# Performance work log

Measured on AMD Instinct MI355X. Metric: run time of the kernel, lower is better.

## Reference

```python
import jax, jax.numpy as jnp
import numpy as np
from jax import lax

LONG_EDGE = 1024
MAX_SIZE = 1333.0
STRIDES = (4, 8, 16, 32, 64)
SIZES = (32, 64, 128, 256, 512)
RATIOS = (0.5, 1.0, 2.0)
PRE_NMS_TOPK = 6000
POST_NMS_TOPK = 1000
NMS_THRESH = 0.7
NUM_CH = 256


def _gen_anchors_level(scale, ratios, shape, stride):
    # faithful copy of generate_anchors_keras (numpy, static)
    scales, ratios = np.meshgrid(np.array([scale], dtype=np.float64), np.array(ratios, dtype=np.float64))
    scales = scales.flatten(); ratios = ratios.flatten()
    size_ratios = stride * stride / ratios
    widths = np.round(np.sqrt(size_ratios))
    heights = np.round(widths * ratios)
    widths = widths * (scales / stride)
    heights = heights * (scales / stride)
    shifts_y = np.arange(0, shape[0]) * stride + (stride - 1) / 2
    shifts_x = np.arange(0, shape[1]) * stride + (stride - 1) / 2
    shifts_x, shifts_y = np.meshgrid(shifts_x, shifts_y)
    box_widths, box_centers_x = np.meshgrid(widths, shifts_x)
    box_heights, box_centers_y = np.meshgrid(heights, shifts_y)
    box_centers = np.stack([box_centers_y, box_centers_x], axis=2).reshape([-1, 2])
    box_sizes = np.stack([box_heights, box_widths], axis=2).reshape([-1, 2])
    boxes = np.concatenate([box_centers - 0.5 * (box_sizes - 1), box_centers + 0.5 * (box_sizes - 1)], axis=1)
    boxes[:, [2, 3]] += 1
    return boxes[:, [1, 0, 3, 2]].astype(np.float32)


def all_anchors():
    shapes = [(int(np.ceil(LONG_EDGE / s)),) * 2 for s in STRIDES]
    return np.concatenate([_gen_anchors_level(SIZES[i], RATIOS, shapes[i], STRIDES[i]) for i in range(len(STRIDES))], axis=0)


def conv2d(x, w, b, padding):
    y = lax.conv_general_dilated(x, w, (1, 1), padding, dimension_numbers=('NCHW', 'OIHW', 'NCHW'))
    return y + b[None, :, None, None]


def decode_bbox_target(deltas, anchors):
    # deltas, anchors: [K,4]
    txty, twth = deltas[:, :2], deltas[:, 2:]
    x1y1, x2y2 = anchors[:, :2], anchors[:, 2:]
    waha = x2y2 - x1y1
    xaya = (x2y2 + x1y1) * 0.5
    clipv = jnp.float32(np.log(MAX_SIZE / 16.0))
    wbhb = jnp.exp(jnp.minimum(twth, clipv)) * waha
    xbyb = txty * waha + xaya
    return jnp.concatenate([xbyb - wbhb * 0.5, xbyb + wbhb * 0.5], axis=1)


def clip_boxes(b, h, w):
    # faithful to source: x clamped to window[0]=h, y to window[1]=w
    return jnp.stack([b[:, 0].clip(0.0, h), b[:, 1].clip(0.0, w), b[:, 2].clip(0.0, h), b[:, 3].clip(0.0, w)], 1)


def nms_keep(boxes, thresh):
    # boxes sorted by descending score; greedy NMS over full IoU matrix
    x1, y1, x2, y2 = boxes[:, 0], boxes[:, 1], boxes[:, 2], boxes[:, 3]
    areas = (x2 - x1) * (y2 - y1)
    iw = jnp.clip(jnp.minimum(x2[:, None], x2[None, :]) - jnp.maximum(x1[:, None], x1[None, :]), 0.0)
    ih = jnp.clip(jnp.minimum(y2[:, None], y2[None, :]) - jnp.maximum(y1[:, None], y1[None, :]), 0.0)
    inter = iw * ih
    iou = inter / (areas[:, None] + areas[None, :] - inter)
    n = boxes.shape[0]
    sup = iou > thresh
    idxs = jnp.arange(n)
    def body(i, keep):
        row = sup[i] & (idxs > i)
        return jnp.where(keep[i], keep & ~row, keep)
    return lax.fori_loop(0, n, body, jnp.ones((n,), bool))


def rpn_forward(image, feats, w0, b0, wcls, bcls, wbox, bbox):
    labels, boxes_l = [], []
    for f in feats:
        hidden = jax.nn.relu(conv2d(f, w0, b0, 'SAME'))
        cls = conv2d(hidden, wcls, bcls, 'VALID')   # [1,A,H,W]
        box = conv2d(hidden, wbox, bbox, 'VALID')   # [1,4A,H,W]
        labels.append(jnp.transpose(cls, (0, 2, 3, 1)).reshape(1, -1, 1))
        boxes_l.append(jnp.transpose(box, (0, 2, 3, 1)).reshape(1, -1, 4))
    scores = jnp.concatenate(labels, axis=1)[0, :, 0]          # [N]
    box_logits = jnp.concatenate(boxes_l, axis=1)[0]           # [N,4]
    anchors = jnp.asarray(all_anchors())                       # [N,4]
    k = min(PRE_NMS_TOPK, anchors.shape[0])
    _, order = lax.top_k(scores, k)
    deltas = box_logits[order]
    pre_anch = anchors[order]
    dec = decode_bbox_target(deltas, pre_anch)
    h, w = float(image.shape[2]), float(image.shape[3])
    boxes = clip_boxes(dec, h, w)
    keep = nms_keep(lax.stop_gradient(boxes), NMS_THRESH)
    sel = jnp.argsort(~keep)[:POST_NMS_TOPK]  # stable: kept boxes in score order, then pad slots
    proposals = jnp.where(keep[sel][:, None], boxes[sel], 0.0)
    return proposals


def setup_inputs() -> dict:
    key = jax.random.key(0)
    ks = jax.random.split(key, 9)
    hw = [256, 128, 64, 32, 16]
    inp = {'image': jax.random.normal(ks[0], (1, 3, 1024, 1024), jnp.float32)}
    for i, s in enumerate(hw):
        inp[f'feat{i}'] = jax.random.normal(jax.random.fold_in(ks[1], i), (1, NUM_CH, s, s), jnp.float32)
    inp['w0'] = jax.random.normal(ks[2], (NUM_CH, NUM_CH, 3, 3), jnp.float32) * 0.01
    inp['b0'] = jnp.zeros((NUM_CH,), jnp.float32)
    inp['wcls'] = jax.random.normal(ks[3], (3, NUM_CH, 1, 1), jnp.float32) * 0.01
    inp['bcls'] = jnp.zeros((3,), jnp.float32)
    inp['wbox'] = jax.random.normal(ks[4], (12, NUM_CH, 1, 1), jnp.float32) * 0.01
    inp['bbox'] = jnp.zeros((12,), jnp.float32)
    return inp


def reference(image, feat0, feat1, feat2, feat3, feat4, w0, b0, wcls, bcls, wbox, bbox):
    feats = [feat0, feat1, feat2, feat3, feat4]
    return rpn_forward(image, feats, w0, b0, wcls, bcls, wbox, bbox)
```

## Files before the change

### kernel.cpp

```cpp
#include <hip/hip_runtime.h>
#include <cstdint>

typedef unsigned long long u64;
typedef unsigned int u32;
typedef unsigned short ushort;
typedef __attribute__((ext_vector_type(8))) short short8;
typedef __attribute__((ext_vector_type(4))) float f32x4;

#define A_TOTAL 261888
#define NPIX    87296
#define KTOP    6000
#define KTARGET 7800
#define NWORDS  94
#define CANDMAX 8192
#define PIXMAX  8192
#define NBINS   16384

__device__ __forceinline__ u64 score_key64(double s) {
  u64 u = (u64)__double_as_longlong(s);
  return (u & 0x8000000000000000ULL) ? ~u : (u | 0x8000000000000000ULL);
}
__device__ __forceinline__ u32 key32(float s) {
  u32 u = __float_as_uint(s);
  return (u & 0x80000000u) ? ~u : (u | 0x80000000u);
}
__device__ __forceinline__ ushort f2bf(float f) {
  u32 u = __float_as_uint(f);
  u32 r = (u + 0x7FFFu + ((u >> 16) & 1u)) >> 16;
  return (ushort)r;
}
__device__ __forceinline__ void pix_level(int pix, int& l, int& off) {
  if (pix < 65536)      { l = 0; off = 0; }
  else if (pix < 81920) { l = 1; off = 65536; }
  else if (pix < 86016) { l = 2; off = 81920; }
  else if (pix < 87040) { l = 3; off = 86016; }
  else                  { l = 4; off = 87040; }
}

__global__ void k_prep_w(const float* __restrict__ w0, double* __restrict__ wt64,
                         ushort* __restrict__ wkf) {
  int i = blockIdx.x * 256 + threadIdx.x;
  if (i < 256 * 2304) {
    int o = i & 255;
    int ictap = i >> 8;
    float v = w0[o * 2304 + ictap];
    wt64[(size_t)ictap * 256 + o] = (double)v;
    int ic = ictap / 9;
    int tap = ictap - ic * 9;
    int w = o >> 6, mt = (o >> 4) & 3, l15 = o & 15;
    int ch = ic >> 5, kk = ic & 31;
    int l4 = kk >> 3, e = kk & 7;
    int lane = l4 * 16 + l15;
    wkf[((((w * 4 + mt) * 8 + ch) * 9 + tap) << 9) + lane * 8 + e] = f2bf(v);
  }
}

__global__ __launch_bounds__(256, 2) void k_conv_mfma(
    const float* __restrict__ f0, const float* __restrict__ f1,
    const float* __restrict__ f2, const float* __restrict__ f3,
    const float* __restrict__ f4,
    const ushort* __restrict__ wkf, const float* __restrict__ b0,
    const float* __restrict__ wcls, const float* __restrict__ bcls,
    float* __restrict__ scr)
{
  __shared__ ushort xsl[100][40];
  __shared__ float  part[3][64][17];

  int b = blockIdx.x;
  int l, tb;
  if (b < 1024)      { l = 0; tb = b; }
  else if (b < 1280) { l = 1; tb = b - 1024; }
  else if (b < 1344) { l = 2; tb = b - 1280; }
  else if (b < 1360) { l = 3; tb = b - 1344; }
  else               { l = 4; tb = b - 1360; }
  const float* feat = (l == 0) ? f0 : (l == 1) ? f1 : (l == 2) ? f2 : (l == 3) ? f3 : f4;
  int Hh = 256 >> l;
  int HW = Hh * Hh;
  int pixOff = (l == 0) ? 0 : (l == 1) ? 65536 : (l == 2) ? 81920 : (l == 3) ? 86016 : 87040;
  int shl = 5 - l;
  int ty = (tb >> shl) << 3;
  int tx = (tb & ((1 << shl) - 1)) << 3;

  int tid = threadIdx.x;
  int w = tid >> 6;
  int lane = tid & 63;
  int l15 = lane & 15;
  int l4 = lane >> 4;

  f32x4 zz = {0.f, 0.f, 0.f, 0.f};
  f32x4 acc[4][4];
  #pragma unroll
  for (int mt = 0; mt < 4; ++mt)
    #pragma unroll
    for (int tt = 0; tt < 4; ++tt) acc[mt][tt] = zz;

  for (int ch = 0; ch < 8; ++ch) {
    __syncthreads();
    for (int e = tid; e < 3200; e += 256) {
      int icl = e / 100;
      int sp = e - icl * 100;
      int yy = sp / 10;
      int xx = sp - yy * 10;
      int gy = ty + yy - 1, gx = tx + xx - 1;
      float v = 0.f;
      if (gy >= 0 && gy < Hh && gx >= 0 && gx < Hh)
        v = feat[(ch * 32 + icl) * HW + gy * Hh + gx];
      xsl[sp][icl] = f2bf(v);
    }
    __syncthreads();
    #pragma unroll
    for (int tap = 0; tap < 9; ++tap) {
      int dy = tap / 3;
      int dx = tap - dy * 3;
      short8 af[4], bf[4];
      #pragma unroll
      for (int mt = 0; mt < 4; ++mt) {
        int abase = ((((w * 4 + mt) * 8 + ch) * 9 + tap) << 9) + (lane << 3);
        af[mt] = *(const short8*)(wkf + abase);
      }
      #pragma unroll
      for (int tt = 0; tt < 4; ++tt) {
        int p = (tt << 4) + l15;
        int sp = ((p >> 3) + dy) * 10 + (p & 7) + dx;
        bf[tt] = *(const short8*)&xsl[sp][l4 << 3];
      }
      #pragma unroll
      for (int mt = 0; mt < 4; ++mt)
        #pragma unroll
        for (int tt = 0; tt < 4; ++tt)
          acc[mt][tt] = __builtin_amdgcn_mfma_f32_16x16x32_bf16(af[mt], bf[tt], acc[mt][tt], 0, 0, 0);
    }
  }

  float pr[3][4];
  #pragma unroll
  for (int kk = 0; kk < 3; ++kk)
    #pragma unroll
    for (int tt = 0; tt < 4; ++tt) pr[kk][tt] = 0.f;
  #pragma unroll
  for (int mt = 0; mt < 4; ++mt) {
    #pragma unroll
    for (int r = 0; r < 4; ++r) {
      int oc = (w << 6) + (mt << 4) + (l4 << 2) + r;
      float bb = b0[oc];
      float c0 = wcls[oc], c1 = wcls[256 + oc], c2 = wcls[512 + oc];
      #pragma unroll
      for (int tt = 0; tt < 4; ++tt) {
        float v = acc[mt][tt][r] + bb;
        v = v > 0.f ? v : 0.f;
        pr[0][tt] = fmaf(c0, v, pr[0][tt]);
        pr[1][tt] = fmaf(c1, v, pr[1][tt]);
        pr[2][tt] = fmaf(c2, v, pr[2][tt]);
      }
    }
  }
  __syncthreads();
  #pragma unroll
  for (int kk = 0; kk < 3; ++kk)
    #pragma unroll
    for (int tt = 0; tt < 4; ++tt)
      part[kk][(tt << 4) + l15][(w << 2) + l4] = pr[kk][tt];
  __syncthreads();
  if (tid < 192) {
    int kk = tid >> 6;
    int px = tid & 63;
    float s = 0.f;
    #pragma unroll
    for (int q = 0; q < 16; ++q) s += part[kk][px][q];
    int pix = pixOff + (ty + (px >> 3)) * Hh + (tx + (px & 7));
    scr[pix * 3 + kk] = s + bcls[kk];
  }
}

__global__ void k_hist1(const float* __restrict__ scr, u32* __restrict__ bins) {
  __shared__ u32 h[NBINS];
  int tid = threadIdx.x;
  for (int idx = tid; idx < NBINS; idx += 256) h[idx] = 0;
  __syncthreads();
  for (int i = blockIdx.x * 256 + tid; i < A_TOTAL; i += gridDim.x * 256)
    atomicAdd(&h[key32(scr[i]) >> 18], 1u);
  __syncthreads();
  for (int idx = tid; idx < NBINS; idx += 256) {
    u32 v = h[idx];
    if (v) atomicAdd(&bins[idx], v);
  }
}

__global__ void k_scan1(const u32* __restrict__ bins, u32* __restrict__ meta) {
  __shared__ u32 psum[256];
  int tid = threadIdx.x;
  u32 s = 0;
  for (int u = 0; u < 64; ++u) s += bins[tid * 64 + u];
  psum[tid] = s;
  __syncthreads();
  if (tid == 0) {
    u32 run = 0;
    for (int t = 255; t >= 0; --t) { u32 tmp = psum[t]; psum[t] = run; run += tmp; }
  }
  __syncthreads();
  u32 cum = psum[tid];
  if (cum < (u32)KTARGET) {
    for (int u = 63; u >= 0; --u) {
      u32 bv = bins[tid * 64 + u];
      u32 nc = cum + bv;
      if (nc >= (u32)KTARGET) {
        meta[0] = (u32)(tid * 64 + u);
        meta[2] = cum;
        break;
      }
      cum = nc;
    }
  }
}

__global__ void k_hist2(const float* __restrict__ scr, const u32* __restrict__ meta,
                        u32* __restrict__ sub) {
  int i = blockIdx.x * 256 + threadIdx.x;
  if (i < A_TOTAL) {
    u32 k = key32(scr[i]);
    if ((k >> 18) == meta[0]) atomicAdd(&sub[(k >> 10) & 0xFFu], 1u);
  }
}

__global__ void k_scan2(const u32* __restrict__ sub, u32* __restrict__ meta) {
  if (threadIdx.x == 0) {
    u32 b = meta[0];
    u32 c = meta[2];
    u32 T = b << 18;
    for (int u = 255; u >= 0; --u) {
      c += sub[u];
      if (c >= (u32)KTARGET) { T = (b << 18) | ((u32)u << 10); break; }
    }
    meta[3] = (T >= (2u << 10)) ? (T - (2u << 10)) : 0u;
  }
}

__global__ void k_cnt2(const float* __restrict__ scr, const u32* __restrict__ meta,
                       u32* __restrict__ blkCnt, u32* __restrict__ blkCntP) {
  __shared__ u32 wc[4], wcp[4];
  int tid = threadIdx.x;
  int lane = tid & 63, wv = tid >> 6;
  u32 T = meta[3];
  int i = blockIdx.x * 256 + tid;
  bool qa = (i < A_TOTAL) && (key32(scr[i]) >= T);
  u64 ba = __ballot(qa);
  bool qp = false;
  if (i < NPIX)
    qp = (key32(scr[i * 3 + 0]) >= T) || (key32(scr[i * 3 + 1]) >= T) || (key32(scr[i * 3 + 2]) >= T);
  u64 bp = __ballot(qp);
  if (lane == 0) { wc[wv] = (u32)__popcll(ba); wcp[wv] = (u32)__popcll(bp); }
  __syncthreads();
  if (tid == 0) {
    blkCnt[blockIdx.x]  = wc[0] + wc[1] + wc[2] + wc[3];
    blkCntP[blockIdx.x] = wcp[0] + wcp[1] + wcp[2] + wcp[3];
  }
}

__global__ __launch_bounds__(1024) void k_scanblk2(const u32* __restrict__ blkCnt,
                                                   u32* __restrict__ blkOff,
                                                   u32* __restrict__ totA,
                                                   const u32* __restrict__ blkCntP,
                                                   u32* __restrict__ blkOffP,
                                                   u32* __restrict__ totP) {
  __shared__ u32 buf[2][1024];
  int tid = threadIdx.x;
  for (int pass = 0; pass < 2; ++pass) {
    const u32* src_ = pass ? blkCntP : blkCnt;
    u32* dst_ = pass ? blkOffP : blkOff;
    u32* tot_ = pass ? totP : totA;
    u32 v = (tid < 1023) ? src_[tid] : 0u;
    buf[0][tid] = v;
    __syncthreads();
    int src = 0;
    for (int d = 1; d < 1024; d <<= 1) {
      u32 t = buf[src][tid] + ((tid >= d) ? buf[src][tid - d] : 0u);
      buf[src ^ 1][tid] = t;
      src ^= 1;
      __syncthreads();
    }
    if (tid < 1023) dst_[tid] = buf[src][tid] - v;
    if (tid == 0) tot_[0] = buf[src][1022];
    __syncthreads();
  }
}

__global__ void k_fill2(const float* __restrict__ scr, const u32* __restrict__ meta,
                        const u32* __restrict__ blkOff, const u32* __restrict__ blkOffP,
                        u32* __restrict__ candIdx, u32* __restrict__ pixList,
                        u32* __restrict__ pixMap) {
  __shared__ u32 wbase[4], wbaseP[4];
  int tid = threadIdx.x;
  int lane = tid & 63, wv = tid >> 6;
  u32 T = meta[3];
  int i = blockIdx.x * 256 + tid;
  bool qa = (i < A_TOTAL) && (key32(scr[i]) >= T);
  u64 ba = __ballot(qa);
  bool qp = false;
  if (i < NPIX)
    qp = (key32(scr[i * 3 + 0]) >= T) || (key32(scr[i * 3 + 1]) >= T) || (key32(scr[i * 3 + 2]) >= T);
  u64 bp = __ballot(qp);
  if (lane == 0) { wbase[wv] = (u32)__popcll(ba); wbaseP[wv] = (u32)__popcll(bp); }
  __syncthreads();
  if (tid == 0) {
    u32 r = blkOff[blockIdx.x];
    #pragma unroll
    for (int w2 = 0; w2 < 4; ++w2) { u32 t = wbase[w2]; wbase[w2] = r; r += t; }
    u32 rp = blkOffP[blockIdx.x];
    #pragma unroll
    for (int w2 = 0; w2 < 4; ++w2) { u32 t = wbaseP[w2]; wbaseP[w2] = rp; rp += t; }
  }
  __syncthreads();
  if (qa) {
    u32 rank = (u32)__popcll(ba & ((1ULL << lane) - 1ULL));
    u32 pos = wbase[wv] + rank;
    if (pos < CANDMAX) candIdx[pos] = (u32)i;
  }
  if (qp) {
    u32 rank = (u32)__popcll(bp & ((1ULL << lane) - 1ULL));
    u32 pos = wbaseP[wv] + rank;
    if (pos < PIXMAX) { pixList[pos] = (u32)i; pixMap[i] = pos; }
  }
}

#define KCH 288
__global__ __launch_bounds__(256, 4) void k_hidden(
    const float* __restrict__ f0, const float* __restrict__ f1,
    const float* __restrict__ f2, const float* __restrict__ f3,
    const float* __restrict__ f4,
    const double* __restrict__ wt64, const float* __restrict__ b0,
    const u32* __restrict__ pixList, const u32* __restrict__ meta,
    double* __restrict__ hbuf)
{
  __shared__ float patch[2][KCH][16];
  __shared__ int sValid[16], sY[16], sX[16], sW[16], sL[16];

  int tid = threadIdx.x;
  int base = blockIdx.x * 16;
  u32 np = meta[4];
  if (np > PIXMAX) np = PIXMAX;
  if (base >= (int)np) return;

  if (tid < 16) {
    int slot = base + tid;
    int v = slot < (int)np;
    sValid[tid] = v;
    int pix = v ? (int)pixList[slot] : 0;
    int l, off;
    pix_level(pix, l, off);
    int W = 256 >> l;
    int idx = pix - off;
    sL[tid] = l;
    sW[tid] = W;
    sY[tid] = idx >> (8 - l);
    sX[tid] = idx & (W - 1);
  }
  __syncthreads();

  auto stage = [&](int cb, int pb) {
    for (int t = tid; t < 1536; t += 256) {
      int s = t & 15;
      int rem = t >> 4;
      int icl = rem / 3;
      int dy = rem - icl * 3;
      int ic = cb * 32 + icl;
      float v0 = 0.f, v1 = 0.f, v2 = 0.f;
      if (sValid[s]) {
        int l = sL[s], W = sW[s], y = sY[s], x = sX[s];
        const float* feat = (l == 0) ? f0 : (l == 1) ? f1 : (l == 2) ? f2 : (l == 3) ? f3 : f4;
        int gy = y + dy - 1;
        if (gy >= 0 && gy < W) {
          const float* rowp = feat + ic * W * W + gy * W;
          if (x - 1 >= 0) v0 = rowp[x - 1];
          v1 = rowp[x];
          if (x + 1 < W) v2 = rowp[x + 1];
        }
      }
      int kb = icl * 9 + dy * 3;
      patch[pb][kb + 0][s] = v0;
      patch[pb][kb + 1][s] = v1;
      patch[pb][kb + 2][s] = v2;
    }
  };

  int ocq = tid & 63;
  int pxq = tid >> 6;

  double acc[4][4];
  #pragma unroll
  for (int i = 0; i < 4; ++i)
    #pragma unroll
    for (int j = 0; j < 4; ++j) acc[i][j] = 0.0;

  stage(0, 0);
  __syncthreads();

  for (int cb = 0; cb < 8; ++cb) {
    if (cb < 7) stage(cb + 1, (cb + 1) & 1);
    const float (*pc)[16] = patch[cb & 1];
    const double* wb_ = wt64 + (size_t)(cb * KCH) * 256 + (ocq << 2);
    for (int kk = 0; kk < KCH; ++kk) {
      float4 p4 = *(const float4*)&pc[kk][pxq << 2];
      double pd0 = (double)p4.x, pd1 = (double)p4.y;
      double pd2 = (double)p4.z, pd3 = (double)p4.w;
      const double* wr = wb_ + (size_t)kk * 256;
      double w0_ = wr[0], w1_ = wr[1], w2_ = wr[2], w3_ = wr[3];
      acc[0][0] = fma(w0_, pd0, acc[0][0]);
      acc[0][1] = fma(w0_, pd1, acc[0][1]);
      acc[0][2] = fma(w0_, pd2, acc[0][2]);
      acc[0][3] = fma(w0_, pd3, acc[0][3]);
      acc[1][0] = fma(w1_, pd0, acc[1][0]);
      acc[1][1] = fma(w1_, pd1, acc[1][1]);
      acc[1][2] = fma(w1_, pd2, acc[1][2]);
      acc[1][3] = fma(w1_, pd3, acc[1][3]);
      acc[2][0] = fma(w2_, pd0, acc[2][0]);
      acc[2][1] = fma(w2_, pd1, acc[2][1]);
      acc[2][2] = fma(w2_, pd2, acc[2][2]);
      acc[2][3] = fma(w2_, pd3, acc[2][3]);
      acc[3][0] = fma(w3_, pd0, acc[3][0]);
      acc[3][1] = fma(w3_, pd1, acc[3][1]);
      acc[3][2] = fma(w3_, pd2, acc[3][2]);
      acc[3][3] = fma(w3_, pd3, acc[3][3]);
    }
    __syncthreads();
  }

  double bb0 = (double)b0[(ocq << 2) + 0];
  double bb1 = (double)b0[(ocq << 2) + 1];
  double bb2 = (double)b0[(ocq << 2) + 2];
  double bb3 = (double)b0[(ocq << 2) + 3];
  #pragma unroll
  for (int j = 0; j < 4; ++j) {
    int s = (pxq << 2) + j;
    if (sValid[s]) {
      double* dst = &hbuf[(size_t)(base + s) * 256 + (ocq << 2)];
      double o0 = acc[0][j] + bb0; dst[0] = o0 > 0.0 ? o0 : 0.0;
      double o1 = acc[1][j] + bb1; dst[1] = o1 > 0.0 ? o1 : 0.0;
      double o2 = acc[2][j] + bb2; dst[2] = o2 > 0.0 ? o2 : 0.0;
      double o3 = acc[3][j] + bb3; dst[3] = o3 > 0.0 ? o3 : 0.0;
    }
  }
}

__global__ __launch_bounds__(256, 4) void k_heads(
    const float* __restrict__ wcls, const float* __restrict__ bcls,
    const float* __restrict__ wbox, const float* __restrict__ bbox,
    const u32* __restrict__ candIdx, const u32* __restrict__ pixMap,
    const u32* __restrict__ meta, const double* __restrict__ hbuf,
    u64* __restrict__ candKey, u32* __restrict__ candPack, double* __restrict__ candDelta)
{
  __shared__ double wavePart[8][5][4];
  __shared__ int sIdx[8], sValid[8], sR[8], sPS[8];
  int tid = threadIdx.x;
  int lane = tid & 63;
  int wv = tid >> 6;
  int base = blockIdx.x * 8;
  u32 cnt = meta[1];
  if (cnt > CANDMAX) cnt = CANDMAX;

  if (base >= (int)cnt) {
    if (tid < 8) {
      candKey[base + tid] = 0ULL;
      candPack[base + tid] = 0xFFFFFFFFu;
    }
    return;
  }

  if (tid < 8) {
    int slot = base + tid;
    int v = slot < (int)cnt;
    sValid[tid] = v;
    int aidx = v ? (int)candIdx[slot] : 0;
    sIdx[tid] = aidx;
    int pix = aidx / 3;
    sR[tid] = aidx - pix * 3;
    sPS[tid] = v ? (int)pixMap[pix] : 0;
  }
  __syncthreads();

  for (int s = 0; s < 8; ++s) {
    if (!sValid[s]) continue;
    int r = sR[s];
    double hv = hbuf[(size_t)sPS[s] * 256 + tid];
    double p0 = (double)wcls[r * 256 + tid] * hv;
    double p1 = (double)wbox[(r * 4 + 0) * 256 + tid] * hv;
    double p2 = (double)wbox[(r * 4 + 1) * 256 + tid] * hv;
    double p3 = (double)wbox[(r * 4 + 2) * 256 + tid] * hv;
    double p4 = (double)wbox[(r * 4 + 3) * 256 + tid] * hv;
    #pragma unroll
    for (int d = 32; d; d >>= 1) {
      p0 += __shfl_xor(p0, d);
      p1 += __shfl_xor(p1, d);
      p2 += __shfl_xor(p2, d);
      p3 += __shfl_xor(p3, d);
      p4 += __shfl_xor(p4, d);
    }
    if (lane == 0) {
      wavePart[s][0][wv] = p0;
      wavePart[s][1][wv] = p1;
      wavePart[s][2][wv] = p2;
      wavePart[s][3][wv] = p3;
      wavePart[s][4][wv] = p4;
    }
  }
  __syncthreads();
  if (tid < 40) {
    int s = tid / 5;
    int k = tid - s * 5;
    int slot = base + s;
    if (sValid[s]) {
      double v = wavePart[s][k][0] + wavePart[s][k][1] + wavePart[s][k][2] + wavePart[s][k][3];
      int r = sR[s];
      if (k == 0) {
        double sc_ = v + (double)bcls[r];
        candKey[slot] = score_key64(sc_);
        candPack[slot] = ((u32)sIdx[s] << 13) | (u32)slot;
      } else {
        candDelta[(size_t)slot * 4 + (k - 1)] = v + (double)bbox[r * 4 + (k - 1)];
      }
    } else if (k == 0) {
      candKey[slot] = 0ULL;
      candPack[slot] = 0xFFFFFFFFu;
    }
  }
}

__global__ __launch_bounds__(256) void k_rank(const u64* __restrict__ candKey,
                                              const u32* __restrict__ candPack,
                                              u32* __restrict__ order) {
  __shared__ u64 fk[1024];
  __shared__ u32 fp[1024];
  __shared__ u32 rsum[32][8];
  int tid = threadIdx.x;
  int c = tid & 31;
  int g = tid >> 5;
  int ci = blockIdx.x * 32 + c;
  u64 mk = candKey[ci];
  u32 mp = candPack[ci];
  u32 cnt = 0;
  for (int chunk = 0; chunk < 8; ++chunk) {
    __syncthreads();
    for (int e = tid; e < 1024; e += 256) {
      fk[e] = candKey[chunk * 1024 + e];
      fp[e] = candPack[chunk * 1024 + e];
    }
    __syncthreads();
    int j0 = g * 128;
    #pragma unroll 4
    for (int j = j0; j < j0 + 128; ++j) {
      u64 kj = fk[j];
      cnt += (kj > mk || (kj == mk && fp[j] < mp)) ? 1u : 0u;
    }
  }
  rsum[c][g] = cnt;
  __syncthreads();
  if (tid < 32) {
    u32 rank = 0;
    #pragma unroll
    for (int q = 0; q < 8; ++q) rank += rsum[tid][q];
    if (rank < (u32)KTOP) order[rank] = mp;
  }
}

__global__ void k_decode(const u32* __restrict__ order, const double* __restrict__ candDelta,
                         double* __restrict__ boxesD) {
  int i = blockIdx.x * 64 + threadIdx.x;
  if (i >= KTOP) return;
  u32 pack = order[i];
  u32 slot = pack & 0x1FFFu;
  u32 a = pack >> 13;
  int pix = (int)(a / 3u);
  int r = (int)(a - (u32)pix * 3u);
  int l, off;
  pix_level(pix, l, off);
  int W = 256 >> l;
  int idx = pix - off;
  int y = idx >> (8 - l);
  int x = idx & (W - 1);
  int s = 4 << l;
  double ratio = (r == 0) ? 0.5 : (r == 1) ? 1.0 : 2.0;
  double wq = rint(sqrt((double)(s * s) / ratio));
  double hq = rint(wq * ratio);
  double Wa = wq * 8.0, Ha = hq * 8.0;
  double cx = (double)x * (double)s + (double)(s - 1) * 0.5;
  double cy = (double)y * (double)s + (double)(s - 1) * 0.5;
  double ax1 = (double)(float)(cx - 0.5 * (Wa - 1.0));
  double ay1 = (double)(float)(cy - 0.5 * (Ha - 1.0));
  double ax2 = (double)(float)(cx + 0.5 * (Wa - 1.0) + 1.0);
  double ay2 = (double)(float)(cy + 0.5 * (Ha - 1.0) + 1.0);
  double tx = candDelta[(size_t)slot * 4 + 0], tyv = candDelta[(size_t)slot * 4 + 1];
  double tw = candDelta[(size_t)slot * 4 + 2], th  = candDelta[(size_t)slot * 4 + 3];
  double wa = ax2 - ax1, ha = ay2 - ay1;
  double xa = (ax1 + ax2) * 0.5, ya = (ay1 + ay2) * 0.5;
  double clipv = (double)(float)log(1333.0 / 16.0);
  double wb = exp(fmin(tw, clipv)) * wa;
  double hb = exp(fmin(th, clipv)) * ha;
  double xb = tx * wa + xa;
  double yb = tyv * ha + ya;
  double bx1 = xb - 0.5 * wb, by1 = yb - 0.5 * hb;
  double bx2 = xb + 0.5 * wb, by2 = yb + 0.5 * hb;
  bx1 = fmin(fmax(bx1, 0.0), 1024.0);
  by1 = fmin(fmax(by1, 0.0), 1024.0);
  bx2 = fmin(fmax(bx2, 0.0), 1024.0);
  by2 = fmin(fmax(by2, 0.0), 1024.0);
  boxesD[(size_t)i * 4 + 0] = bx1;
  boxesD[(size_t)i * 4 + 1] = by1;
  boxesD[(size_t)i * 4 + 2] = bx2;
  boxesD[(size_t)i * 4 + 3] = by2;
}

__global__ void k_mask(const double* __restrict__ boxesD, u64* __restrict__ maskA) {
  __shared__ double cbx[64][4];
  int lane = threadIdx.x;
  int bc = blockIdx.x, br = blockIdx.y;
  if (bc < br) return;
  int ci = bc * 64 + lane;
  if (ci < KTOP) {
    cbx[lane][0] = boxesD[(size_t)ci * 4 + 0];
    cbx[lane][1] = boxesD[(size_t)ci * 4 + 1];
    cbx[lane][2] = boxesD[(size_t)ci * 4 + 2];
    cbx[lane][3] = boxesD[(size_t)ci * 4 + 3];
  } else {
    cbx[lane][0] = -1e30; cbx[lane][1] = -1e30; cbx[lane][2] = -1e30; cbx[lane][3] = -1e30;
  }
  __syncthreads();
  int ri = br * 64 + lane;
  if (ri >= KTOP) return;
  double rx1 = boxesD[(size_t)ri * 4 + 0], ry1 = boxesD[(size_t)ri * 4 + 1];
  double rx2 = boxesD[(size_t)ri * 4 + 2], ry2 = boxesD[(size_t)ri * 4 + 3];
  double ra = (rx2 - rx1) * (ry2 - ry1);
  u64 bits = 0;
  #pragma unroll 4
  for (int j = 0; j < 64; ++j) {
    int cj = bc * 64 + j;
    double iw = fmin(rx2, cbx[j][2]) - fmax(rx1, cbx[j][0]);
    double ih = fmin(ry2, cbx[j][3]) - fmax(ry1, cbx[j][1]);
    iw = fmax(iw, 0.0); ih = fmax(ih, 0.0);
    double inter = iw * ih;
    double ca = (cbx[j][2] - cbx[j][0]) * (cbx[j][3] - cbx[j][1]);
    double iou = inter / (ra + ca - inter);
    if (cj > ri && iou > 0.7) bits |= (1ULL << j);
  }
  maskA[(size_t)ri * NWORDS + bc] = bits;
}

__global__ __launch_bounds__(1024) void k_nms_reduce(const u64* __restrict__ maskA,
                                                     u32* __restrict__ keep) {
  __shared__ u64 rm[NWORDS];
  int tid = threadIdx.x;
  int wv = tid >> 6, lane = tid & 63;
  for (int i = tid; i < NWORDS; i += 1024) rm[i] = 0ULL;
  __syncthreads();
  u64 diagNext = maskA[(size_t)lane * NWORDS + 0];
  int keptTot = 0;
  for (int c = 0; c < NWORDS; ++c) {
    int rows = KTOP - c * 64; if (rows > 64) rows = 64;
    u64 validM = (rows == 64) ? ~0ULL : ((1ULL << rows) - 1ULL);
    size_t rowbase = (size_t)(c * 64 + lane) * NWORDS;
    bool lv = lane < rows;
    int w0i = c + wv;
    u64 v0 = (lv && w0i      < NWORDS) ? maskA[rowbase + w0i]      : 0ULL;
    u64 v1 = (lv && w0i + 16 < NWORDS) ? maskA[rowbase + w0i + 16] : 0ULL;
    u64 v2 = (lv && w0i + 32 < NWORDS) ? maskA[rowbase + w0i + 32] : 0ULL;
    u64 v3 = (lv && w0i + 48 < NWORDS) ? maskA[rowbase + w0i + 48] : 0ULL;
    u64 v4 = (lv && w0i + 64 < NWORDS) ? maskA[rowbase + w0i + 64] : 0ULL;
    u64 v5 = (lv && w0i + 80 < NWORDS) ? maskA[rowbase + w0i + 80] : 0ULL;
    u64 diag = diagNext;
    if (c + 1 < NWORDS) {
      int nrows = KTOP - (c + 1) * 64; if (nrows > 64) nrows = 64;
      diagNext = (lane < nrows) ? maskA[(size_t)((c + 1) * 64 + lane) * NWORDS + (c + 1)] : 0ULL;
    }
    u64 R = rm[c];
    u64 undec = (~R) & validM;
    u64 km = 0;
    while (undec) {
      int j = __builtin_ctzll(undec);
      km |= (1ULL << j);
      u64 dj = (u64)__shfl((unsigned long long)diag, j);
      undec &= ~(dj | (1ULL << j));
    }
    if (wv == 0 && lane < rows) keep[c * 64 + lane] = (u32)((km >> lane) & 1ULL);
    keptTot += (int)__popcll(km);
    if (keptTot >= 1000) {
      for (int i = (c + 1) * 64 + tid; i < KTOP; i += 1024) keep[i] = 0u;
      return;
    }
    u64 sel = ((km >> lane) & 1ULL) ? ~0ULL : 0ULL;
    v0 &= sel; v1 &= sel; v2 &= sel; v3 &= sel; v4 &= sel; v5 &= sel;
    #pragma unroll
    for (int s = 32; s; s >>= 1) {
      v0 |= (u64)__shfl_xor((unsigned long long)v0, s);
      v1 |= (u64)__shfl_xor((unsigned long long)v1, s);
      v2 |= (u64)__shfl_xor((unsigned long long)v2, s);
      v3 |= (u64)__shfl_xor((unsigned long long)v3, s);
      v4 |= (u64)__shfl_xor((unsigned long long)v4, s);
      v5 |= (u64)__shfl_xor((unsigned long long)v5, s);
    }
    if (lane == 0) {
      if (w0i      < NWORDS) rm[w0i]      |= v0;
      if (w0i + 16 < NWORDS) rm[w0i + 16] |= v1;
      if (w0i + 32 < NWORDS) rm[w0i + 32] |= v2;
      if (w0i + 48 < NWORDS) rm[w0i + 48] |= v3;
      if (w0i + 64 < NWORDS) rm[w0i + 64] |= v4;
      if (w0i + 80 < NWORDS) rm[w0i + 80] |= v5;
    }
    __syncthreads();
  }
}

__global__ __launch_bounds__(1024) void k_emit(const u32* __restrict__ keep,
                                               const double* __restrict__ boxesD,
                                               float* __restrict__ out) {
  __shared__ u32 partial[1024];
  __shared__ u32 excl[1024];
  int tid = threadIdx.x;
  for (int j = tid; j < 4000; j += 1024) out[j] = 0.f;
  int base = tid * 6;
  u32 kv[6];
  u32 c = 0;
  #pragma unroll
  for (int u = 0; u < 6; ++u) {
    int j = base + u;
    kv[u] = (j < KTOP) ? keep[j] : 0u;
    c += kv[u];
  }
  partial[tid] = c;
  __syncthreads();
  if (tid == 0) {
    u32 run = 0;
    for (int t = 0; t < 1024; ++t) { excl[t] = run; run += partial[t]; }
  }
  __syncthreads();
  u32 p = excl[tid];
  #pragma unroll
  for (int u = 0; u < 6; ++u) {
    int j = base + u;
    if (j < KTOP && kv[u]) {
      if (p < 1000u) {
        out[p * 4 + 0] = (float)boxesD[(size_t)j * 4 + 0];
        out[p * 4 + 1] = (float)boxesD[(size_t)j * 4 + 1];
        out[p * 4 + 2] = (float)boxesD[(size_t)j * 4 + 2];
        out[p * 4 + 3] = (float)boxesD[(size_t)j * 4 + 3];
      }
      ++p;
    }
  }
}

extern "C" void kernel_launch(void* const* d_in, const int* in_sizes, int n_in,
                              void* d_out, int out_size, void* d_ws, size_t ws_size,
                              hipStream_t stream) {
  const float* f0   = (const float*)d_in[1];
  const float* f1   = (const float*)d_in[2];
  const float* f2   = (const float*)d_in[3];
  const float* f3   = (const float*)d_in[4];
  const float* f4   = (const float*)d_in[5];
  const float* w0   = (const float*)d_in[6];
  const float* b0   = (const float*)d_in[7];
  const float* wcls = (const float*)d_in[8];
  const float* bcls = (const float*)d_in[9];
  const float* wbox = (const float*)d_in[10];
  const float* bbox = (const float*)d_in[11];
  float* out = (float*)d_out;
  char* ws = (char*)d_ws;

  size_t off = 0;
  auto alloc = [&](size_t bytes) { size_t o = off; off += (bytes + 255) & ~(size_t)255; return o; };
  size_t off_scr  = alloc((size_t)A_TOTAL * 4);
  size_t off_w64  = alloc((size_t)256 * 2304 * 8);
  size_t off_wk   = alloc((size_t)256 * 2304 * 2);
  size_t off_hb   = alloc((size_t)PIXMAX * 256 * 8);
  size_t off_ci   = alloc((size_t)CANDMAX * 4);
  size_t off_ck   = alloc((size_t)CANDMAX * 8);
  size_t off_cp   = alloc((size_t)CANDMAX * 4);
  size_t off_cd   = alloc((size_t)CANDMAX * 4 * 8);
  size_t off_pl   = alloc((size_t)PIXMAX * 4);
  size_t off_pm   = alloc((size_t)NPIX * 4);
  size_t off_box  = alloc((size_t)KTOP * 4 * 8);
  size_t off_ord  = alloc((size_t)KTOP * 4);
  size_t off_keep = alloc((size_t)KTOP * 4);
  size_t off_mask = alloc((size_t)KTOP * NWORDS * 8);
  size_t off_bcnt = alloc((size_t)1024 * 4);
  size_t off_boff = alloc((size_t)1024 * 4);
  size_t off_bcp  = alloc((size_t)1024 * 4);
  size_t off_bop  = alloc((size_t)1024 * 4);
  size_t off_bins = alloc((size_t)NBINS * 4);
  size_t off_sub  = alloc((size_t)256 * 4);
  size_t off_meta = alloc((size_t)64 * 4);
  size_t off_end  = off;
  (void)in_sizes; (void)n_in; (void)out_size; (void)ws_size;

  float*  scr       = (float*)(ws + off_scr);
  double* wt64      = (double*)(ws + off_w64);
  ushort* wkf       = (ushort*)(ws + off_wk);
  double* hbuf      = (double*)(ws + off_hb);
  u32*    candIdx   = (u32*)(ws + off_ci);
  u64*    candKey   = (u64*)(ws + off_ck);
  u32*    candPack  = (u32*)(ws + off_cp);
  double* candDelta = (double*)(ws + off_cd);
  u32*    pixList   = (u32*)(ws + off_pl);
  u32*    pixMap    = (u32*)(ws + off_pm);
  double* boxesD    = (double*)(ws + off_box);
  u32*    order     = (u32*)(ws + off_ord);
  u32*    keep      = (u32*)(ws + off_keep);
  u64*    maskA     = (u64*)(ws + off_mask);
  u32*    blkCnt    = (u32*)(ws + off_bcnt);
  u32*    blkOff    = (u32*)(ws + off_boff);
  u32*    blkCntP   = (u32*)(ws + off_bcp);
  u32*    blkOffP   = (u32*)(ws + off_bop);
  u32*    bins      = (u32*)(ws + off_bins);
  u32*    sub       = (u32*)(ws + off_sub);
  u32*    meta      = (u32*)(ws + off_meta);

  hipMemsetAsync(ws + off_bins, 0, off_end - off_bins, stream);

  k_prep_w<<<2304, 256, 0, stream>>>(w0, wt64, wkf);
  k_conv_mfma<<<1364, 256, 0, stream>>>(f0, f1, f2, f3, f4, wkf, b0, wcls, bcls, scr);
  k_hist1<<<64, 256, 0, stream>>>(scr, bins);
  k_scan1<<<1, 256, 0, stream>>>(bins, meta);
  k_hist2<<<1023, 256, 0, stream>>>(scr, meta, sub);
  k_scan2<<<1, 64, 0, stream>>>(sub, meta);
  k_cnt2<<<1023, 256, 0, stream>>>(scr, meta, blkCnt, blkCntP);
  k_scanblk2<<<1, 1024, 0, stream>>>(blkCnt, blkOff, meta + 1, blkCntP, blkOffP, meta + 4);
  k_fill2<<<1023, 256, 0, stream>>>(scr, meta, blkOff, blkOffP, candIdx, pixList, pixMap);
  k_hidden<<<PIXMAX / 16, 256, 0, stream>>>(f0, f1, f2, f3, f4, wt64, b0, pixList, meta, hbuf);
  k_heads<<<CANDMAX / 8, 256, 0, stream>>>(wcls, bcls, wbox, bbox, candIdx, pixMap, meta, hbuf,
                                           candKey, candPack, candDelta);
  k_rank<<<CANDMAX / 32, 256, 0, stream>>>(candKey, candPack, order);
  k_decode<<<94, 64, 0, stream>>>(order, candDelta, boxesD);
  k_mask<<<dim3(NWORDS, NWORDS), 64, 0, stream>>>(boxesD, maskA);
  k_nms_reduce<<<1, 1024, 0, stream>>>(maskA, keep);
  k_emit<<<1, 1024, 0, stream>>>(keep, boxesD, out);
}
```

Baseline: 894.3 us.

## Stage conv weights through LDS with register-prefetched double buffering

The hidden 3x3 conv kernel used to read its fp64 weights straight from global memory in the inner loop. It now loads a 16-row chunk of weights into registers one step ahead, commits it to a shared-memory tile, and has the FMA loop read weights from LDS. The goal is to cut repeated global/L2 weight traffic and latency. In exchange it adds two block barriers per 16-k group, needs 32KB of extra LDS, holds 16 prefetch registers, and lowers launch bounds to 2 blocks per SM.

Result: slower. 1.121 ms (+25.3%).

```diff
diff --git a/kernel.cpp b/kernel.cpp
--- a/kernel.cpp
+++ b/kernel.cpp
@@ -323,7 +323,9 @@
 }
 
 #define KCH 288
-__global__ __launch_bounds__(256, 4) void k_hidden(
+#define WG  16
+#define NGRP (KCH / WG)
+__global__ __launch_bounds__(256, 2) void k_hidden(
     const float* __restrict__ f0, const float* __restrict__ f1,
     const float* __restrict__ f2, const float* __restrict__ f3,
     const float* __restrict__ f4,
@@ -331,6 +333,7 @@
     const u32* __restrict__ pixList, const u32* __restrict__ meta,
     double* __restrict__ hbuf)
 {
+  __shared__ double wlds[WG * 256];
   __shared__ float patch[2][KCH][16];
   __shared__ int sValid[16], sY[16], sX[16], sW[16], sL[16];
 
@@ -384,6 +387,20 @@
 
   int ocq = tid & 63;
   int pxq = tid >> 6;
+  int wkk = tid >> 4;
+  int woc = (tid & 15) << 4;
+
+  double wpre[16];
+  auto wload = [&](int gk0) {
+    const double* src = wt64 + (size_t)(gk0 + wkk) * 256 + woc;
+    #pragma unroll
+    for (int j = 0; j < 16; ++j) wpre[j] = src[j];
+  };
+  auto wcommit = [&]() {
+    double* dst = &wlds[wkk * 256 + woc];
+    #pragma unroll
+    for (int j = 0; j < 16; ++j) dst[j] = wpre[j];
+  };
 
   double acc[4][4];
   #pragma unroll
@@ -392,36 +409,46 @@
     for (int j = 0; j < 4; ++j) acc[i][j] = 0.0;
 
   stage(0, 0);
-  __syncthreads();
-
+  wload(0);
+  __syncthreads();
+  wcommit();
+  __syncthreads();
+
+  int gAbs = 0;
   for (int cb = 0; cb < 8; ++cb) {
     if (cb < 7) stage(cb + 1, (cb + 1) & 1);
     const float (*pc)[16] = patch[cb & 1];
-    const double* wb_ = wt64 + (size_t)(cb * KCH) * 256 + (ocq << 2);
-    for (int kk = 0; kk < KCH; ++kk) {
-      float4 p4 = *(const float4*)&pc[kk][pxq << 2];
-      double pd0 = (double)p4.x, pd1 = (double)p4.y;
-      double pd2 = (double)p4.z, pd3 = (double)p4.w;
-      const double* wr = wb_ + (size_t)kk * 256;
-      double w0_ = wr[0], w1_ = wr[1], w2_ = wr[2], w3_ = wr[3];
-      acc[0][0] = fma(w0_, pd0, acc[0][0]);
-      acc[0][1] = fma(w0_, pd1, acc[0][1]);
-      acc[0][2] = fma(w0_, pd2, acc[0][2]);
-      acc[0][3] = fma(w0_, pd3, acc[0][3]);
-      acc[1][0] = fma(w1_, pd0, acc[1][0]);
-      acc[1][1] = fma(w1_, pd1, acc[1][1]);
-      acc[1][2] = fma(w1_, pd2, acc[1][2]);
-      acc[1][3] = fma(w1_, pd3, acc[1][3]);
-      acc[2][0] = fma(w2_, pd0, acc[2][0]);
-      acc[2][1] = fma(w2_, pd1, acc[2][1]);
-      acc[2][2] = fma(w2_, pd2, acc[2][2]);
-      acc[2][3] = fma(w2_, pd3, acc[2][3]);
-      acc[3][0] = fma(w3_, pd0, acc[3][0]);
-      acc[3][1] = fma(w3_, pd1, acc[3][1]);
-      acc[3][2] = fma(w3_, pd2, acc[3][2]);
-      acc[3][3] = fma(w3_, pd3, acc[3][3]);
-    }
-    __syncthreads();
+    for (int g = 0; g < NGRP; ++g, ++gAbs) {
+      bool more = (gAbs + 1) < 8 * NGRP;
+      if (more) wload((gAbs + 1) * WG);
+      int kbase = g * WG;
+      for (int kk = 0; kk < WG; ++kk) {
+        float4 p4 = *(const float4*)&pc[kbase + kk][pxq << 2];
+        double pd0 = (double)p4.x, pd1 = (double)p4.y;
+        double pd2 = (double)p4.z, pd3 = (double)p4.w;
+        const double* wr = &wlds[kk * 256 + (ocq << 2)];
+        double w0_ = wr[0], w1_ = wr[1], w2_ = wr[2], w3_ = wr[3];
+        acc[0][0] = fma(w0_, pd0, acc[0][0]);
+        acc[0][1] = fma(w0_, pd1, acc[0][1]);
+        acc[0][2] = fma(w0_, pd2, acc[0][2]);
+        acc[0][3] = fma(w0_, pd3, acc[0][3]);
+        acc[1][0] = fma(w1_, pd0, acc[1][0]);
+        acc[1][1] = fma(w1_, pd1, acc[1][1]);
+        acc[1][2] = fma(w1_, pd2, acc[1][2]);
+        acc[1][3] = fma(w1_, pd3, acc[1][3]);
+        acc[2][0] = fma(w2_, pd0, acc[2][0]);
+        acc[2][1] = fma(w2_, pd1, acc[2][1]);
+        acc[2][2] = fma(w2_, pd2, acc[2][2]);
+        acc[2][3] = fma(w2_, pd3, acc[2][3]);
+        acc[3][0] = fma(w3_, pd0, acc[3][0]);
+        acc[3][1] = fma(w3_, pd1, acc[3][1]);
+        acc[3][2] = fma(w3_, pd2, acc[3][2]);
+        acc[3][3] = fma(w3_, pd3, acc[3][3]);
+      }
+      __syncthreads();
+      if (more) wcommit();
+      __syncthreads();
+    }
   }
 
   double bb0 = (double)b0[(ocq << 2) + 0];
```

## Split hidden conv reduction over two K-halves with a combine kernel

Applied to the files above, without the earlier changes.

The FP64 hidden-layer conv for the selected pixels is split along the input-channel reduction into two halves, doubling the block count, with each half writing partial sums to a new workspace buffer. A new combine kernel adds the two partials, applies bias and ReLU, and writes the hidden buffer. This aims to fill more CUs when few pixel blocks exist. The cost is an extra kernel launch and roughly 2x16MB of partial-sum traffic. Summation order changes slightly.

Measured after the change: 900.0 us. Within noise of the previous version (+0.6%).

```diff
diff --git a/kernel.cpp b/kernel.cpp
--- a/kernel.cpp
+++ b/kernel.cpp
@@ -327,15 +327,17 @@
     const float* __restrict__ f0, const float* __restrict__ f1,
     const float* __restrict__ f2, const float* __restrict__ f3,
     const float* __restrict__ f4,
-    const double* __restrict__ wt64, const float* __restrict__ b0,
+    const double* __restrict__ wt64,
     const u32* __restrict__ pixList, const u32* __restrict__ meta,
-    double* __restrict__ hbuf)
+    double* __restrict__ hpart)
 {
   __shared__ float patch[2][KCH][16];
   __shared__ int sValid[16], sY[16], sX[16], sW[16], sL[16];
 
   int tid = threadIdx.x;
-  int base = blockIdx.x * 16;
+  int pixblk = blockIdx.x >> 1;
+  int kc = blockIdx.x & 1;
+  int base = pixblk * 16;
   u32 np = meta[4];
   if (np > PIXMAX) np = PIXMAX;
   if (base >= (int)np) return;
@@ -391,12 +393,14 @@
     #pragma unroll
     for (int j = 0; j < 4; ++j) acc[i][j] = 0.0;
 
-  stage(0, 0);
-  __syncthreads();
-
-  for (int cb = 0; cb < 8; ++cb) {
-    if (cb < 7) stage(cb + 1, (cb + 1) & 1);
-    const float (*pc)[16] = patch[cb & 1];
+  int cb0 = kc * 4;
+  stage(cb0, 0);
+  __syncthreads();
+
+  for (int i = 0; i < 4; ++i) {
+    int cb = cb0 + i;
+    if (i < 3) stage(cb + 1, (i + 1) & 1);
+    const float (*pc)[16] = patch[i & 1];
     const double* wb_ = wt64 + (size_t)(cb * KCH) * 256 + (ocq << 2);
     for (int kk = 0; kk < KCH; ++kk) {
       float4 p4 = *(const float4*)&pc[kk][pxq << 2];
@@ -424,21 +428,30 @@
     __syncthreads();
   }
 
-  double bb0 = (double)b0[(ocq << 2) + 0];
-  double bb1 = (double)b0[(ocq << 2) + 1];
-  double bb2 = (double)b0[(ocq << 2) + 2];
-  double bb3 = (double)b0[(ocq << 2) + 3];
   #pragma unroll
   for (int j = 0; j < 4; ++j) {
     int s = (pxq << 2) + j;
     if (sValid[s]) {
-      double* dst = &hbuf[(size_t)(base + s) * 256 + (ocq << 2)];
-      double o0 = acc[0][j] + bb0; dst[0] = o0 > 0.0 ? o0 : 0.0;
-      double o1 = acc[1][j] + bb1; dst[1] = o1 > 0.0 ? o1 : 0.0;
-      double o2 = acc[2][j] + bb2; dst[2] = o2 > 0.0 ? o2 : 0.0;
-      double o3 = acc[3][j] + bb3; dst[3] = o3 > 0.0 ? o3 : 0.0;
-    }
-  }
+      double* dst = &hpart[((size_t)kc * PIXMAX + base + s) * 256 + (ocq << 2)];
+      dst[0] = acc[0][j];
+      dst[1] = acc[1][j];
+      dst[2] = acc[2][j];
+      dst[3] = acc[3][j];
+    }
+  }
+}
+
+__global__ void k_combine(const double* __restrict__ hpart, const float* __restrict__ b0,
+                          const u32* __restrict__ meta, double* __restrict__ hbuf) {
+  int b = blockIdx.x;
+  u32 np = meta[4];
+  if (np > PIXMAX) np = PIXMAX;
+  if (b >= (int)np) return;
+  int tid = threadIdx.x;
+  double p0 = hpart[(size_t)b * 256 + tid];
+  double p1 = hpart[((size_t)PIXMAX + b) * 256 + tid];
+  double t = (p0 + p1) + (double)b0[tid];
+  hbuf[(size_t)b * 256 + tid] = t > 0.0 ? t : 0.0;
 }
 
 __global__ __launch_bounds__(256, 4) void k_heads(
@@ -769,6 +782,7 @@
   size_t off_w64  = alloc((size_t)256 * 2304 * 8);
   size_t off_wk   = alloc((size_t)256 * 2304 * 2);
   size_t off_hb   = alloc((size_t)PIXMAX * 256 * 8);
+  size_t off_hp   = alloc((size_t)2 * PIXMAX * 256 * 8);
   size_t off_ci   = alloc((size_t)CANDMAX * 4);
   size_t off_ck   = alloc((size_t)CANDMAX * 8);
   size_t off_cp   = alloc((size_t)CANDMAX * 4);
@@ -793,6 +807,7 @@
   double* wt64      = (double*)(ws + off_w64);
   ushort* wkf       = (ushort*)(ws + off_wk);
   double* hbuf      = (double*)(ws + off_hb);
+  double* hpart     = (double*)(ws + off_hp);
   u32*    candIdx   = (u32*)(ws + off_ci);
   u64*    candKey   = (u64*)(ws + off_ck);
   u32*    candPack  = (u32*)(ws + off_cp);
@@ -822,7 +837,8 @@
   k_cnt2<<<1023, 256, 0, stream>>>(scr, meta, blkCnt, blkCntP);
   k_scanblk2<<<1, 1024, 0, stream>>>(blkCnt, blkOff, meta + 1, blkCntP, blkOffP, meta + 4);
   k_fill2<<<1023, 256, 0, stream>>>(scr, meta, blkOff, blkOffP, candIdx, pixList, pixMap);
-  k_hidden<<<PIXMAX / 16, 256, 0, stream>>>(f0, f1, f2, f3, f4, wt64, b0, pixList, meta, hbuf);
+  k_hidden<<<(PIXMAX / 16) * 2, 256, 0, stream>>>(f0, f1, f2, f3, f4, wt64, pixList, meta, hpart);
+  k_combine<<<PIXMAX, 256, 0, stream>>>(hpart, b0, meta, hbuf);
   k_heads<<<CANDMAX / 8, 256, 0, stream>>>(wcls, bcls, wbox, bbox, candIdx, pixMap, meta, hbuf,
                                            candKey, candPack, candDelta);
   k_rank<<<CANDMAX / 32, 256, 0, stream>>>(candKey, candPack, order);
```
